# Kernel optimization log

Measured on AMD Instinct MI355X. Metric: run time of the kernel, lower is better.

Reference implementation:

```python
import jax, jax.numpy as jnp
import numpy as np

B, T, C = 4, 2048, 1024
WIN = 16


def setup_inputs() -> dict:
    key = jax.random.key(0)
    ks = jax.random.split(key, 5)
    s = 1.0 / np.sqrt(C)
    return {
        "x": jax.random.normal(ks[0], (B, T, C), dtype=jnp.float32),
        "Wq": jax.random.normal(ks[1], (C, C), dtype=jnp.float32) * s,
        "bq": jnp.zeros((C,), jnp.float32),
        "Wk": jax.random.normal(ks[2], (C, C), dtype=jnp.float32) * s,
        "bk": jnp.zeros((C,), jnp.float32),
        "Wv": jax.random.normal(ks[3], (C, C), dtype=jnp.float32) * s,
        "bv": jnp.zeros((C,), jnp.float32),
        "Wo": jax.random.normal(ks[4], (C, C), dtype=jnp.float32) * s,
        "bo": jnp.zeros((C,), jnp.float32),
        "window": WIN,
    }


def reference(x, Wq, bq, Wk, bk, Wv, bv, Wo, bo, window):
    Bn, Tn, Cn = x.shape
    half = window // 2
    W = 2 * half + 1  # keys per query (window [t-half, t+half])
    q = x @ Wq.T + bq
    k = x @ Wk.T + bk
    v = x @ Wv.T + bv
    offs = jnp.arange(-half, half + 1)              # [W]
    tpos = jnp.arange(Tn)                            # [T]
    idx = tpos[:, None] + offs[None, :]              # [T, W]
    valid = (idx >= 0) & (idx < Tn)                  # [T, W]
    idx_c = jnp.clip(idx, 0, Tn - 1)
    k_win = k[:, idx_c, :]                           # [B, T, W, C]
    v_win = v[:, idx_c, :]                           # [B, T, W, C]
    scale = 1.0 / jnp.sqrt(jnp.asarray(Cn, x.dtype))
    scores = jnp.einsum('btc,btwc->btw', q, k_win) * scale
    scores = jnp.where(valid[None, :, :], scores, jnp.finfo(x.dtype).min)
    attn = jax.nn.softmax(scores, axis=-1)           # [B, T, W]
    ctx = jnp.einsum('btw,btwc->btc', attn, v_win)   # [B, T, C]
    return ctx @ Wo.T + bo
```

## Files before the change

kernel.cpp:

```cpp
#include <hip/hip_runtime.h>
#include <cstdint>
#include <cstddef>

#define B_ 4
#define T_ 2048
#define C_ 1024
#define M_ (B_ * T_)
#define HALF_ 8
#define W_ 17
#define NT 32

typedef unsigned short u16;
typedef _Float16 half8 __attribute__((ext_vector_type(8)));
typedef float f32x16 __attribute__((ext_vector_type(16)));
typedef unsigned short ushort8v __attribute__((ext_vector_type(8)));

__device__ __forceinline__ ushort4 cvt4(float4 v) {
    ushort4 o;
    _Float16 a = (_Float16)v.x; o.x = __builtin_bit_cast(unsigned short, a);
    _Float16 b = (_Float16)v.y; o.y = __builtin_bit_cast(unsigned short, b);
    _Float16 c = (_Float16)v.z; o.z = __builtin_bit_cast(unsigned short, c);
    _Float16 d = (_Float16)v.w; o.w = __builtin_bit_cast(unsigned short, d);
    return o;
}


__global__ void prologue2(const float* __restrict__ x,
                          const float* __restrict__ Wq, const float* __restrict__ Wk,
                          const float* __restrict__ Wv, const float* __restrict__ Wo,
                          const float* __restrict__ bq, const float* __restrict__ bk,
                          const float* __restrict__ bv,
                          u16* __restrict__ xf, u16* __restrict__ wfq,
                          u16* __restrict__ wfo, float* __restrict__ bcat) {
    const int blk = blockIdx.x;
    const int tid = threadIdx.x;
    if (blk >= 3072) {
        int i = (blk - 3072) * 256 + tid;
        const float* src = (i < 1024) ? bq : (i < 2048) ? bk : bv;
        bcat[i] = src[i & 1023];
        return;
    }
    __shared__ ushort8v g16[512];
    const float* src;
    u16* dst;
    size_t chunk_base;
    int kg;
    if (blk < 2048) {
        const int mt = blk >> 3; kg = blk & 7;
        src = x + (size_t)mt * 32 * C_;
        dst = xf; chunk_base = (size_t)mt * 64;
    } else {
        const int w = blk - 2048;
        const int mat = w >> 8, nt = (w >> 3) & 31; kg = w & 7;
        src = ((mat == 0) ? Wq : (mat == 1) ? Wk : (mat == 2) ? Wv : Wo)
              + (size_t)nt * 32 * C_;
        if (mat < 3) { dst = wfq; chunk_base = (size_t)(mat * 32 + nt) * 64; }
        else         { dst = wfo; chunk_base = (size_t)nt * 64; }
    }
    const int r = tid >> 3, gc = (tid & 7) * 2;
    const float4* s4 = (const float4*)(src + (size_t)r * C_ + kg * 128 + (tid & 7) * 16);
    float4 f0 = s4[0], f1 = s4[1], f2 = s4[2], f3 = s4[3];
    ushort4 h0 = cvt4(f0), h1 = cvt4(f1), h2 = cvt4(f2), h3 = cvt4(f3);
    ushort8v ga, gb;
    ga[0]=h0.x; ga[1]=h0.y; ga[2]=h0.z; ga[3]=h0.w;
    ga[4]=h1.x; ga[5]=h1.y; ga[6]=h1.z; ga[7]=h1.w;
    gb[0]=h2.x; gb[1]=h2.y; gb[2]=h2.z; gb[3]=h2.w;
    gb[4]=h3.x; gb[5]=h3.y; gb[6]=h3.z; gb[7]=h3.w;
    g16[r * 16 + ((gc    ) ^ (r & 15))] = ga;
    g16[r * 16 + ((gc + 1) ^ (r & 15))] = gb;
    __syncthreads();
    const int lane = tid & 63, rr = lane & 31, hi = lane >> 5;
#pragma unroll
    for (int r2 = 0; r2 < 2; ++r2) {
        const int ksl = r2 * 4 + (tid >> 6);
        const int g = ksl * 2 + hi;
        ushort8v v = g16[rr * 16 + (g ^ (rr & 15))];
        *(ushort8v*)(dst + ((chunk_base + kg * 8 + ksl) * 64 + lane) * 8) = v;
    }
}


#define AS1_ __attribute__((address_space(1)))
#define AS3_ __attribute__((address_space(3)))

__device__ __forceinline__ void gload16(const u16* g, u16* l) {
    __builtin_amdgcn_global_load_lds((AS1_ void*)g, (AS3_ void*)l, 16, 0, 0);
}

#define MFMA_ __builtin_amdgcn_mfma_f32_32x32x16_f16

#define STAGE(NB, KT) { const size_t ko = (size_t)(KT) * 1024;            \
    gload16(gA0 + ko, (NB) + lA0); gload16(gA1 + ko, (NB) + lA1);         \
    gload16(gA2 + ko, (NB) + lA2); gload16(gA3 + ko, (NB) + lA3);         \
    gload16(gB0 + ko, (NB) + lB0); gload16(gB1 + ko, (NB) + lB1); }

#define TILE(CB, NB, KT, DOSTG, VW)                                        \
  {                                                                        \
    half8 a0 = *(const half8*)((CB) + oA);                                 \
    half8 a1 = *(const half8*)((CB) + oA + 1024);                          \
    half8 a2 = *(const half8*)((CB) + oA + 2048);                          \
    half8 a3 = *(const half8*)((CB) + oA + 3072);                          \
    half8 b0v = *(const half8*)((CB) + oB);                                \
    half8 b1v = *(const half8*)((CB) + oB + 1024);                         \
    if (DOSTG) STAGE(NB, (KT) + 2);                                        \
    __builtin_amdgcn_s_setprio(1);                                         \
    acc00 = MFMA_(a0, b0v, acc00, 0, 0, 0);                                \
    acc01 = MFMA_(a0, b1v, acc01, 0, 0, 0);                                \
    acc10 = MFMA_(a1, b0v, acc10, 0, 0, 0);                                \
    acc11 = MFMA_(a1, b1v, acc11, 0, 0, 0);                                \
    acc20 = MFMA_(a2, b0v, acc20, 0, 0, 0);                                \
    acc21 = MFMA_(a2, b1v, acc21, 0, 0, 0);                                \
    acc30 = MFMA_(a3, b0v, acc30, 0, 0, 0);                                \
    acc31 = MFMA_(a3, b1v, acc31, 0, 0, 0);                                \
    __builtin_amdgcn_s_setprio(0);                                         \
    a0 = *(const half8*)((CB) + oA + 512);                                 \
    a1 = *(const half8*)((CB) + oA + 1536);                                \
    a2 = *(const half8*)((CB) + oA + 2560);                                \
    a3 = *(const half8*)((CB) + oA + 3584);                                \
    b0v = *(const half8*)((CB) + oB + 512);                                \
    b1v = *(const half8*)((CB) + oB + 1536);                               \
    __builtin_amdgcn_s_setprio(1);                                         \
    acc00 = MFMA_(a0, b0v, acc00, 0, 0, 0);                                \
    acc01 = MFMA_(a0, b1v, acc01, 0, 0, 0);                                \
    acc10 = MFMA_(a1, b0v, acc10, 0, 0, 0);                                \
    acc11 = MFMA_(a1, b1v, acc11, 0, 0, 0);                                \
    acc20 = MFMA_(a2, b0v, acc20, 0, 0, 0);                                \
    acc21 = MFMA_(a2, b1v, acc21, 0, 0, 0);                                \
    acc30 = MFMA_(a3, b0v, acc30, 0, 0, 0);                                \
    acc31 = MFMA_(a3, b1v, acc31, 0, 0, 0);                                \
    __builtin_amdgcn_s_setprio(0);                                         \
    if ((VW) == 6)      asm volatile("s_waitcnt vmcnt(6) lgkmcnt(0)" ::: "memory"); \
    else if ((VW) == 0) asm volatile("s_waitcnt vmcnt(0) lgkmcnt(0)" ::: "memory"); \
    else                asm volatile("s_waitcnt lgkmcnt(0)" ::: "memory"); \
    asm volatile("s_barrier" ::: "memory");                                \
  }

__global__ __launch_bounds__(256, 2) void gemm_qkv(
    const u16* __restrict__ Afrag, const u16* __restrict__ Bfrag,
    const float* __restrict__ bias, u16* __restrict__ qkvf)
{
    __shared__ u16 lds[3][12288];
    const int tid  = threadIdx.x;
    const int lane = tid & 63;
    const int wave = tid >> 6;
    const int wm   = wave >> 1;
    const int wn   = wave & 1;
    const int la8  = lane * 8;

    const int nb  = gridDim.x * gridDim.y;
    int bid = blockIdx.y * gridDim.x + blockIdx.x;
    bid = (bid & 7) * (nb >> 3) + (bid >> 3);
    const int bx = bid % gridDim.x;
    const int by = bid / gridDim.x;

    const u16* gA0 = Afrag + ((size_t)(by*8 + ((wave    )>>1))*64 + ((wave    )&1))*512 + la8;
    const u16* gA1 = Afrag + ((size_t)(by*8 + ((wave+ 4 )>>1))*64 + ((wave+ 4 )&1))*512 + la8;
    const u16* gA2 = Afrag + ((size_t)(by*8 + ((wave+ 8 )>>1))*64 + ((wave+ 8 )&1))*512 + la8;
    const u16* gA3 = Afrag + ((size_t)(by*8 + ((wave+12 )>>1))*64 + ((wave+12 )&1))*512 + la8;
    const u16* gB0 = Bfrag + ((size_t)(bx*4 + ((wave    )>>1))*64 + ((wave    )&1))*512 + la8;
    const u16* gB1 = Bfrag + ((size_t)(bx*4 + ((wave+ 4 )>>1))*64 + ((wave+ 4 )&1))*512 + la8;
    const int lA0 = (wave     ) * 512;
    const int lA1 = (wave +  4) * 512;
    const int lA2 = (wave +  8) * 512;
    const int lA3 = (wave + 12) * 512;
    const int lB0 = 8192 + (wave    ) * 512;
    const int lB1 = 8192 + (wave + 4) * 512;

    const int oA = wm * 4096 + la8;
    const int oB = 8192 + wn * 2048 + la8;

    u16* b0 = &lds[0][0];
    u16* b1 = &lds[1][0];
    u16* b2 = &lds[2][0];

    STAGE(b0, 0);
    STAGE(b1, 1);
    asm volatile("s_waitcnt vmcnt(6)" ::: "memory");
    asm volatile("s_barrier" ::: "memory");

    f32x16 acc00, acc01, acc10, acc11, acc20, acc21, acc30, acc31;
#pragma unroll
    for (int r = 0; r < 16; ++r) {
        acc00[r] = 0.f; acc01[r] = 0.f; acc10[r] = 0.f; acc11[r] = 0.f;
        acc20[r] = 0.f; acc21[r] = 0.f; acc30[r] = 0.f; acc31[r] = 0.f;
    }

#pragma unroll 1
    for (int kt = 0; kt < NT - 2; kt += 3) {
        TILE(b0, b2, kt,     1, 6);
        TILE(b1, b0, kt + 1, 1, 6);
        TILE(b2, b1, kt + 2, 1, 6);
    }
    TILE(b0, b2, NT - 2, 0, 0);
    TILE(b1, b2, NT - 1, 0, -1);

    const int m0 = by * 256 + wm * 128;
    const int n0 = bx * 128 + wn * 64;
    f32x16 accs[4][2] = {{acc00, acc01}, {acc10, acc11}, {acc20, acc21}, {acc30, acc31}};
#pragma unroll
    for (int i = 0; i < 4; ++i) {
#pragma unroll
        for (int j = 0; j < 2; ++j) {
            const int col = n0 + j * 32 + (lane & 31);
            const int mat = col >> 10;
            const int ch  = col & 1023;
            const float bv = bias[col];
            u16* dst = qkvf + (size_t)mat * ((size_t)M_ * C_);
#pragma unroll
            for (int reg = 0; reg < 16; ++reg) {
                const int m = m0 + i * 32 + (reg & 3) + 8 * (reg >> 2) + 4 * (lane >> 5);
                _Float16 h = (_Float16)(accs[i][j][reg] + bv);
                size_t addr;
                if (mat < 2) {
                    addr = (size_t)((m >> 5) * 64 + (ch >> 4)) * 512
                         + ((m & 31) + 32 * ((ch >> 3) & 1)) * 8 + (ch & 7);
                } else {
                    addr = (size_t)((m >> 4) * 32 + (ch >> 5)) * 512
                         + ((ch & 31) + 32 * ((m >> 3) & 1)) * 8 + (m & 7);
                }
                dst[addr] = __builtin_bit_cast(unsigned short, h);
            }
        }
    }
}

#define STAGE_S0(NB, KO) { gload16(gA0 + (KO), (NB) + lsA0); gload16(gB0 + (KO), (NB) + lsB0); }
#define STAGE_S1(NB, KO) { gload16(gA1 + (KO), (NB) + lsA1); gload16(gB1 + (KO), (NB) + lsB1); }

#define TILE_S(CB, NB, KT, DOSTG, VW)                                      \
  {                                                                        \
    const size_t ko = (size_t)((KT) + 2) * 1024;                           \
    half8 a0 = *(const half8*)((CB) + oA);                                 \
    half8 a1 = *(const half8*)((CB) + oA + 1024);                          \
    half8 b0v = *(const half8*)((CB) + oB);                                \
    half8 b1v = *(const half8*)((CB) + oB + 1024);                         \
    if (DOSTG) STAGE_S0(NB, ko);                                           \
    __builtin_amdgcn_s_setprio(1);                                         \
    acc00 = MFMA_(a0, b0v, acc00, 0, 0, 0);                                \
    acc01 = MFMA_(a0, b1v, acc01, 0, 0, 0);                                \
    acc10 = MFMA_(a1, b0v, acc10, 0, 0, 0);                                \
    acc11 = MFMA_(a1, b1v, acc11, 0, 0, 0);                                \
    __builtin_amdgcn_s_setprio(0);                                         \
    a0 = *(const half8*)((CB) + oA + 512);                                 \
    a1 = *(const half8*)((CB) + oA + 1536);                                \
    b0v = *(const half8*)((CB) + oB + 512);                                \
    b1v = *(const half8*)((CB) + oB + 1536);                               \
    if (DOSTG) STAGE_S1(NB, ko);                                           \
    __builtin_amdgcn_s_setprio(1);                                         \
    acc00 = MFMA_(a0, b0v, acc00, 0, 0, 0);                                \
    acc01 = MFMA_(a0, b1v, acc01, 0, 0, 0);                                \
    acc10 = MFMA_(a1, b0v, acc10, 0, 0, 0);                                \
    acc11 = MFMA_(a1, b1v, acc11, 0, 0, 0);                                \
    __builtin_amdgcn_s_setprio(0);                                         \
    if ((VW) == 4)      asm volatile("s_waitcnt vmcnt(4) lgkmcnt(0)" ::: "memory"); \
    else if ((VW) == 0) asm volatile("s_waitcnt vmcnt(0) lgkmcnt(0)" ::: "memory"); \
    else                asm volatile("s_waitcnt lgkmcnt(0)" ::: "memory"); \
    asm volatile("s_barrier" ::: "memory");                                \
  }

__global__ __launch_bounds__(256, 2) void gemm_s(
    const u16* __restrict__ Afrag, const u16* __restrict__ Bfrag,
    const float* __restrict__ bias, float* __restrict__ Cout, int Ndim)
{
    __shared__ u16 lds[3][8192];
    const int tid  = threadIdx.x;
    const int lane = tid & 63;
    const int wave = tid >> 6;
    const int wm   = wave >> 1;
    const int wn   = wave & 1;
    const int la8  = lane * 8;

    const int nb  = gridDim.x * gridDim.y;
    int bid = blockIdx.y * gridDim.x + blockIdx.x;
    bid = (bid & 7) * (nb >> 3) + (bid >> 3);
    const int bx = bid % gridDim.x;
    const int by = bid / gridDim.x;

    const u16* gA0 = Afrag + ((size_t)(by*4 + ((wave    )>>1))*64 + ((wave    )&1))*512 + la8;
    const u16* gA1 = Afrag + ((size_t)(by*4 + ((wave+ 4 )>>1))*64 + ((wave+ 4 )&1))*512 + la8;
    const u16* gB0 = Bfrag + ((size_t)(bx*4 + ((wave    )>>1))*64 + ((wave    )&1))*512 + la8;
    const u16* gB1 = Bfrag + ((size_t)(bx*4 + ((wave+ 4 )>>1))*64 + ((wave+ 4 )&1))*512 + la8;
    const int lsA0 = (wave    ) * 512;
    const int lsA1 = (wave + 4) * 512;
    const int lsB0 = 4096 + (wave    ) * 512;
    const int lsB1 = 4096 + (wave + 4) * 512;

    const int oA = wm * 2048 + la8;
    const int oB = 4096 + wn * 2048 + la8;

    u16* b0 = &lds[0][0];
    u16* b1 = &lds[1][0];
    u16* b2 = &lds[2][0];

    STAGE_S0(b0, 0); STAGE_S1(b0, 0);
    STAGE_S0(b1, 1024); STAGE_S1(b1, 1024);
    asm volatile("s_waitcnt vmcnt(4)" ::: "memory");
    asm volatile("s_barrier" ::: "memory");

    f32x16 acc00, acc01, acc10, acc11;
#pragma unroll
    for (int r = 0; r < 16; ++r) { acc00[r] = 0.f; acc01[r] = 0.f; acc10[r] = 0.f; acc11[r] = 0.f; }

#pragma unroll 1
    for (int kt = 0; kt < NT - 2; kt += 3) {
        TILE_S(b0, b2, kt,     1, 4);
        TILE_S(b1, b0, kt + 1, 1, 4);
        TILE_S(b2, b1, kt + 2, 1, 4);
    }
    TILE_S(b0, b2, NT - 2, 0, 0);
    TILE_S(b1, b2, NT - 1, 0, -1);

    const int m0 = by * 128 + wm * 64;
    const int n0 = bx * 128 + wn * 64;
    f32x16 accs[2][2] = {{acc00, acc01}, {acc10, acc11}};
#pragma unroll
    for (int i = 0; i < 2; ++i) {
#pragma unroll
        for (int j = 0; j < 2; ++j) {
            const int col = n0 + j * 32 + (lane & 31);
            const float bv = bias[col];
#pragma unroll
            for (int reg = 0; reg < 16; ++reg) {
                const int row = m0 + i * 32 + (reg & 3) + 8 * (reg >> 2) + 4 * (lane >> 5);
                Cout[(size_t)row * Ndim + col] = accs[i][j][reg] + bv;
            }
        }
    }
}

__global__ __launch_bounds__(64) void attn_mfma(
    const u16* __restrict__ qf, const u16* __restrict__ kf,
    const u16* __restrict__ vf, u16* __restrict__ ctxf)
{
    const int l   = threadIdx.x;
    const int q   = l & 31;
    const int hi  = l >> 5;
    const int t0  = blockIdx.x * 32;
    const int t0l = t0 & (T_ - 1);

    const int r1 = min(max(t0 - 16 + q, 0), M_ - 1);
    const int r2 = min(max(t0 + 16 + q, 0), M_ - 1);
    const u16* a1p = kf + (size_t)(r1 >> 5) * 32768 + ((r1 & 31) + 32 * hi) * 8;
    const u16* a2p = kf + (size_t)(r2 >> 5) * 32768 + ((r2 & 31) + 32 * hi) * 8;
    const u16* qp  = qf + (size_t)(t0 >> 5) * 32768 + l * 8;

    f32x16 sc1, sc2;
#pragma unroll
    for (int r = 0; r < 16; ++r) { sc1[r] = 0.f; sc2[r] = 0.f; }
#pragma unroll 8
    for (int ks = 0; ks < 64; ++ks) {
        half8 a1 = *(const half8*)(a1p + ks * 512);
        half8 a2 = *(const half8*)(a2p + ks * 512);
        half8 qb = *(const half8*)(qp  + ks * 512);
        sc1 = MFMA_(a1, qb, sc1, 0, 0, 0);
        sc2 = MFMA_(a2, qb, sc2, 0, 0, 0);
    }

    float px1[16], px2[16];
#pragma unroll
    for (int r = 0; r < 16; ++r) {
        px1[r] = __shfl_xor(sc1[r], 32);
        px2[r] = __shfl_xor(sc2[r], 32);
    }

    const int plo = max(q + 8, 16 - t0l);
    const int phi = min(q + 24, (T_ + 15) - t0l);
    float s[64];
#pragma unroll
    for (int p = 0; p < 64; ++p) {
        const int row = p & 31;
        const int h   = (row >> 2) & 1;
        const int rg  = (row & 3) + 4 * (row >> 3);
        const float own = (p < 32) ? sc1[rg] : sc2[rg];
        const float oth = (p < 32) ? px1[rg] : px2[rg];
        const float v = (h == hi) ? own : oth;
        s[p] = (p >= plo && p <= phi) ? v * 0.03125f : -3.0e38f;
    }

    float mx = s[0];
#pragma unroll
    for (int p = 1; p < 64; ++p) mx = fmaxf(mx, s[p]);
    float den = 0.f;
#pragma unroll
    for (int p = 0; p < 64; ++p) { const float w = __expf(s[p] - mx); s[p] = w; den += w; }
    const float inv = 1.f / den;

    half8 pa0, pa1, pa2, pa3;
#pragma unroll
    for (int e = 0; e < 8; ++e) {
        pa0[e] = (_Float16)((hi ? s[ 8 + e] : s[ 0 + e]) * inv);
        pa1[e] = (_Float16)((hi ? s[24 + e] : s[16 + e]) * inv);
        pa2[e] = (_Float16)((hi ? s[40 + e] : s[32 + e]) * inv);
        pa3[e] = (_Float16)((hi ? s[56 + e] : s[48 + e]) * inv);
    }

    const int s0i = (t0 - 16) >> 4;
    const u16* vb0p = vf + (size_t)min(max(s0i    , 0), M_/16 - 1) * 16384 + l * 8;
    const u16* vb1p = vf + (size_t)min(max(s0i + 1, 0), M_/16 - 1) * 16384 + l * 8;
    const u16* vb2p = vf + (size_t)min(max(s0i + 2, 0), M_/16 - 1) * 16384 + l * 8;
    const u16* vb3p = vf + (size_t)min(max(s0i + 3, 0), M_/16 - 1) * 16384 + l * 8;
    const size_t ctxb = (size_t)(t0 >> 5) * 32768;
    const int lpo = 32 * ((l >> 3) & 1);
    const int e7  = l & 7;
#pragma unroll 2
    for (int n = 0; n < 32; ++n) {
        half8 v0 = *(const half8*)(vb0p + n * 512);
        half8 v1 = *(const half8*)(vb1p + n * 512);
        half8 v2 = *(const half8*)(vb2p + n * 512);
        half8 v3 = *(const half8*)(vb3p + n * 512);
        f32x16 o;
#pragma unroll
        for (int r = 0; r < 16; ++r) o[r] = 0.f;
        o = MFMA_(pa0, v0, o, 0, 0, 0);
        o = MFMA_(pa1, v1, o, 0, 0, 0);
        o = MFMA_(pa2, v2, o, 0, 0, 0);
        o = MFMA_(pa3, v3, o, 0, 0, 0);
        u16* cp = ctxf + ctxb + (size_t)(2 * n + (q >> 4)) * 512 + e7;
#pragma unroll
        for (int r = 0; r < 16; ++r) {
            const int mrow = (r & 3) + 8 * (r >> 2) + 4 * hi;
            _Float16 hv = (_Float16)o[r];
            cp[(mrow + lpo) * 8] = __builtin_bit_cast(unsigned short, hv);
        }
    }
}

extern "C" void kernel_launch(void* const* d_in, const int* in_sizes, int n_in,
                              void* d_out, int out_size, void* d_ws, size_t ws_size,
                              hipStream_t stream) {
    const float* x  = (const float*)d_in[0];
    const float* Wq = (const float*)d_in[1];
    const float* bq = (const float*)d_in[2];
    const float* Wk = (const float*)d_in[3];
    const float* bk = (const float*)d_in[4];
    const float* Wv = (const float*)d_in[5];
    const float* bv = (const float*)d_in[6];
    const float* Wo = (const float*)d_in[7];
    const float* bo = (const float*)d_in[8];
    float* out = (float*)d_out;

    const size_t MC = (size_t)M_ * C_;
    u16* xf   = (u16*)d_ws;
    u16* wfq  = xf   + MC;
    u16* wfo  = wfq  + 3 * (size_t)C_ * C_;
    u16* qkvf = wfo  + (size_t)C_ * C_;
    u16* ctxf = qkvf + 3 * MC;
    float* bcat = (float*)(ctxf + MC);

    prologue2<<<3084, 256, 0, stream>>>(x, Wq, Wk, Wv, Wo, bq, bk, bv,
                                        xf, wfq, wfo, bcat);

    dim3 gqkv(3072 / 128, M_ / 256);
    gemm_qkv<<<gqkv, 256, 0, stream>>>(xf, wfq, bcat, qkvf);

    attn_mfma<<<M_ / 32, 64, 0, stream>>>(qkvf, qkvf + MC, qkvf + 2 * MC, ctxf);

    dim3 go(C_ / 128, M_ / 128);
    gemm_s<<<go, 256, 0, stream>>>(ctxf, wfo, bo, out, C_);
}
```

Measured before the change: 253.1 us.

## Store QKV row-major and add separate V reformat kernel before attention

The QKV GEMM epilogue now writes a plain row-major [M,3072] fp16 matrix instead of scattering into MFMA-fragment layouts. A new vfmt kernel transposes V into the fragment layout, reusing the x workspace buffer. The attention kernel then reads Q and K directly from the row-major buffer with strided per-row loads. This simplifies the GEMM epilogue stores but adds a kernel launch and an extra pass over V. The attention K/Q loads become less coalesced.

```diff
diff --git a/kernel.cpp b/kernel.cpp
--- a/kernel.cpp
+++ b/kernel.cpp
@@ -6,8 +6,7 @@
 #define T_ 2048
 #define C_ 1024
 #define M_ (B_ * T_)
-#define HALF_ 8
-#define W_ 17
+#define QKV_STRIDE 3072
 #define NT 32
 
 typedef unsigned short u16;
@@ -79,7 +78,6 @@
     }
 }
 
-
 #define AS1_ __attribute__((address_space(1)))
 #define AS3_ __attribute__((address_space(3)))
 
@@ -88,6 +86,7 @@
 }
 
 #define MFMA_ __builtin_amdgcn_mfma_f32_32x32x16_f16
+#define LD8_(p) (*(const half8*)(p))
 
 #define STAGE(NB, KT) { const size_t ko = (size_t)(KT) * 1024;            \
     gload16(gA0 + ko, (NB) + lA0); gload16(gA1 + ko, (NB) + lA1);         \
@@ -135,9 +134,9 @@
     asm volatile("s_barrier" ::: "memory");                                \
   }
 
-__global__ __launch_bounds__(256, 2) void gemm_qkv(
+__global__ __launch_bounds__(256, 2) void gemm_p2(
     const u16* __restrict__ Afrag, const u16* __restrict__ Bfrag,
-    const float* __restrict__ bias, u16* __restrict__ qkvf)
+    const float* __restrict__ bias, u16* __restrict__ Cout, int Ndim)
 {
     __shared__ u16 lds[3][12288];
     const int tid  = threadIdx.x;
@@ -202,23 +201,12 @@
 #pragma unroll
         for (int j = 0; j < 2; ++j) {
             const int col = n0 + j * 32 + (lane & 31);
-            const int mat = col >> 10;
-            const int ch  = col & 1023;
             const float bv = bias[col];
-            u16* dst = qkvf + (size_t)mat * ((size_t)M_ * C_);
 #pragma unroll
             for (int reg = 0; reg < 16; ++reg) {
-                const int m = m0 + i * 32 + (reg & 3) + 8 * (reg >> 2) + 4 * (lane >> 5);
+                const int row = m0 + i * 32 + (reg & 3) + 8 * (reg >> 2) + 4 * (lane >> 5);
                 _Float16 h = (_Float16)(accs[i][j][reg] + bv);
-                size_t addr;
-                if (mat < 2) {
-                    addr = (size_t)((m >> 5) * 64 + (ch >> 4)) * 512
-                         + ((m & 31) + 32 * ((ch >> 3) & 1)) * 8 + (ch & 7);
-                } else {
-                    addr = (size_t)((m >> 4) * 32 + (ch >> 5)) * 512
-                         + ((ch & 31) + 32 * ((m >> 3) & 1)) * 8 + (m & 7);
-                }
-                dst[addr] = __builtin_bit_cast(unsigned short, h);
+                Cout[(size_t)row * Ndim + col] = __builtin_bit_cast(unsigned short, h);
             }
         }
     }
@@ -328,9 +316,42 @@
     }
 }
 
-__global__ __launch_bounds__(64) void attn_mfma(
-    const u16* __restrict__ qf, const u16* __restrict__ kf,
-    const u16* __restrict__ vf, u16* __restrict__ ctxf)
+__global__ __launch_bounds__(256) void vfmt(
+    const u16* __restrict__ qkv, u16* __restrict__ vf)
+{
+    __shared__ ushort8v g16[512];
+    const int blk = blockIdx.x;
+    const int tid = threadIdx.x;
+    const int tb = blk >> 3, cb = blk & 7;
+    const int r = tid >> 3;
+    const int gc = (tid & 7) * 2;
+    const u16* src = qkv + (size_t)(tb * 32 + r) * QKV_STRIDE + 2048 + cb * 128 + (tid & 7) * 16;
+    ushort8v ga = *(const ushort8v*)src;
+    ushort8v gb = *(const ushort8v*)(src + 8);
+    g16[r * 16 + ((gc    ) ^ (r & 15))] = ga;
+    g16[r * 16 + ((gc + 1) ^ (r & 15))] = gb;
+    __syncthreads();
+    const int lane = tid & 63, wave = tid >> 6, hi = lane >> 5;
+#pragma unroll
+    for (int r2 = 0; r2 < 2; ++r2) {
+        const int k = wave + 4 * r2;
+        const int cl = (k & 3) * 32 + (lane & 31);
+        const int gi = cl >> 3, sub = cl & 7;
+        const int tbase = 16 * (k >> 2) + 8 * hi;
+        ushort8v outv;
+#pragma unroll
+        for (int e = 0; e < 8; ++e) {
+            const int tl = tbase + e;
+            outv[e] = ((const u16*)&g16[tl * 16 + (gi ^ (tl & 15))])[sub];
+        }
+        const size_t chunk = (size_t)tb * 64 + (k >> 2) * 32 + cb * 4 + (k & 3);
+        *(ushort8v*)(vf + chunk * 512 + lane * 8) = outv;
+    }
+}
+
+__global__ __launch_bounds__(64) void attn_rm(
+    const u16* __restrict__ qkv, const u16* __restrict__ vf,
+    u16* __restrict__ ctxf)
 {
     const int l   = threadIdx.x;
     const int q   = l & 31;
@@ -340,18 +361,18 @@
 
     const int r1 = min(max(t0 - 16 + q, 0), M_ - 1);
     const int r2 = min(max(t0 + 16 + q, 0), M_ - 1);
-    const u16* a1p = kf + (size_t)(r1 >> 5) * 32768 + ((r1 & 31) + 32 * hi) * 8;
-    const u16* a2p = kf + (size_t)(r2 >> 5) * 32768 + ((r2 & 31) + 32 * hi) * 8;
-    const u16* qp  = qf + (size_t)(t0 >> 5) * 32768 + l * 8;
+    const u16* a1p = qkv + (size_t)r1 * QKV_STRIDE + 1024 + hi * 8;
+    const u16* a2p = qkv + (size_t)r2 * QKV_STRIDE + 1024 + hi * 8;
+    const u16* qp  = qkv + (size_t)(t0 + q) * QKV_STRIDE + hi * 8;
 
     f32x16 sc1, sc2;
 #pragma unroll
     for (int r = 0; r < 16; ++r) { sc1[r] = 0.f; sc2[r] = 0.f; }
 #pragma unroll 8
     for (int ks = 0; ks < 64; ++ks) {
-        half8 a1 = *(const half8*)(a1p + ks * 512);
-        half8 a2 = *(const half8*)(a2p + ks * 512);
-        half8 qb = *(const half8*)(qp  + ks * 512);
+        half8 a1 = LD8_(a1p + ks * 16);
+        half8 a2 = LD8_(a2p + ks * 16);
+        half8 qb = LD8_(qp  + ks * 16);
         sc1 = MFMA_(a1, qb, sc1, 0, 0, 0);
         sc2 = MFMA_(a2, qb, sc2, 0, 0, 0);
     }
@@ -404,10 +425,10 @@
     const int e7  = l & 7;
 #pragma unroll 2
     for (int n = 0; n < 32; ++n) {
-        half8 v0 = *(const half8*)(vb0p + n * 512);
-        half8 v1 = *(const half8*)(vb1p + n * 512);
-        half8 v2 = *(const half8*)(vb2p + n * 512);
-        half8 v3 = *(const half8*)(vb3p + n * 512);
+        half8 v0 = LD8_(vb0p + n * 512);
+        half8 v1 = LD8_(vb1p + n * 512);
+        half8 v2 = LD8_(vb2p + n * 512);
+        half8 v3 = LD8_(vb3p + n * 512);
         f32x16 o;
 #pragma unroll
         for (int r = 0; r < 16; ++r) o[r] = 0.f;
@@ -443,17 +464,20 @@
     u16* xf   = (u16*)d_ws;
     u16* wfq  = xf   + MC;
     u16* wfo  = wfq  + 3 * (size_t)C_ * C_;
-    u16* qkvf = wfo  + (size_t)C_ * C_;
-    u16* ctxf = qkvf + 3 * MC;
+    u16* qkvh = wfo  + (size_t)C_ * C_;
+    u16* ctxf = qkvh + (size_t)M_ * QKV_STRIDE;
     float* bcat = (float*)(ctxf + MC);
+    u16* vf   = xf;
 
     prologue2<<<3084, 256, 0, stream>>>(x, Wq, Wk, Wv, Wo, bq, bk, bv,
                                         xf, wfq, wfo, bcat);
 
-    dim3 gqkv(3072 / 128, M_ / 256);
-    gemm_qkv<<<gqkv, 256, 0, stream>>>(xf, wfq, bcat, qkvf);
-
-    attn_mfma<<<M_ / 32, 64, 0, stream>>>(qkvf, qkvf + MC, qkvf + 2 * MC, ctxf);
+    dim3 gqkv(QKV_STRIDE / 128, M_ / 256);
+    gemm_p2<<<gqkv, 256, 0, stream>>>(xf, wfq, bcat, qkvh, QKV_STRIDE);
+
+    vfmt<<<2048, 256, 0, stream>>>(qkvh, vf);
+
+    attn_rm<<<M_ / 32, 64, 0, stream>>>(qkvh, vf, ctxf);
 
     dim3 go(C_ / 128, M_ / 128);
     gemm_s<<<go, 256, 0, stream>>>(ctxf, wfo, bo, out, C_);
```

New measurement: 233.2 us. 1.09x faster.
